# Kernel optimization log

Hardware: AMD Instinct MI355X
Metric: run time of the kernel (lower is better)

The kernel has to match this reference:

```python
import jax, jax.numpy as jnp
import numpy as np

RATIO, NH, NG, KS, RF, UP = 4, 2, 2, 3, 11.0, 2


def _cln(t, g, b):
    # channel-wise LayerNorm on NCHW (LayerNormProxy), eps=1e-5
    mu = t.mean(axis=1, keepdims=True)
    var = ((t - mu) ** 2).mean(axis=1, keepdims=True)
    return (t - mu) * jax.lax.rsqrt(var + 1e-5) * g[None, :, None, None] + b[None, :, None, None]


def _resize_ac(img, oH, oW):
    # bilinear resize, align_corners=True (F.interpolate)
    H, W = img.shape[-2], img.shape[-1]
    ys = jnp.arange(oH, dtype=img.dtype) * ((H - 1) / (oH - 1))
    y0 = jnp.clip(jnp.floor(ys), 0, H - 2).astype(jnp.int32)
    wy = ys - y0.astype(img.dtype)
    xs = jnp.arange(oW, dtype=img.dtype) * ((W - 1) / (oW - 1))
    x0 = jnp.clip(jnp.floor(xs), 0, W - 2).astype(jnp.int32)
    wx = xs - x0.astype(img.dtype)
    t = img[..., y0, :] * (1.0 - wy)[:, None] + img[..., y0 + 1, :] * wy[:, None]
    return t[..., x0] * (1.0 - wx) + t[..., x0 + 1] * wx


def _grid_sample(img, iy, ix):
    # bilinear grid_sample, padding_mode='zeros', align_corners=True
    # img [Bg,Cx,H,W]; iy,ix [Bg,N] unnormalized input-pixel coords
    H, W = img.shape[-2], img.shape[-1]
    def one(im, yy, xx):
        y0f, x0f = jnp.floor(yy), jnp.floor(xx)
        wy, wx = yy - y0f, xx - x0f
        y0, x0 = y0f.astype(jnp.int32), x0f.astype(jnp.int32)
        def gat(yi, xi):
            valid = ((yi >= 0) & (yi < H) & (xi >= 0) & (xi < W)).astype(im.dtype)
            return im[:, jnp.clip(yi, 0, H - 1), jnp.clip(xi, 0, W - 1)] * valid[None]
        return (gat(y0, x0) * ((1 - wy) * (1 - wx))[None]
                + gat(y0, x0 + 1) * ((1 - wy) * wx)[None]
                + gat(y0 + 1, x0) * (wy * (1 - wx))[None]
                + gat(y0 + 1, x0 + 1) * (wy * wx)[None])
    return jax.vmap(one)(img, iy, ix)


def _conv2d(x, w, groups=1):
    return jax.lax.conv_general_dilated(x, w, (1, 1), 'SAME', feature_group_count=groups,
                                        dimension_numbers=('NCHW', 'OIHW', 'NCHW'))


def _forward(x, ln_g, ln_b, Wq, Wk, dw_w, off_ln_g, off_ln_b, off_w, off_b, rpb):
    B, C, H, W = x.shape
    hidden = C // RATIO
    gc = hidden // NG
    c2 = hidden // NH          # attn_dim per head
    oH, oW = int(H * UP), int(W * UP)
    N1, n = oH * oW, KS * KS
    scale = c2 ** -0.5
    v = x
    xn = _cln(x, ln_g, ln_b)
    q = jnp.einsum('oc,bchw->bohw', Wq, xn)
    k = jnp.einsum('oc,bchw->bohw', Wk, xn)
    q = _resize_ac(q, oH, oW)                        # [B,hidden,oH,oW]
    # offset prediction
    q_off = q.reshape(B * NG, gc, oH, oW)
    t = _conv2d(q_off, dw_w, groups=gc)
    t = _cln(t, off_ln_g, off_ln_b)
    t = jax.nn.gelu(t, approximate=False)
    pred = _conv2d(t, off_w) + off_b[None, :, None, None]  # [Bg,2*ks^2,oH,oW]
    pad = (KS - 1) // 2
    rng = jnp.arange(-pad, pad + 1, dtype=x.dtype)
    base = jnp.stack(jnp.meshgrid(rng, rng, indexing='ij'), axis=-1)  # [KS,KS,2] (y,x)
    off = jnp.tanh(pred).reshape(B * NG, KS, KS, 2, oH, oW) * RF + base[None, :, :, :, None, None]
    py = off[:, :, :, 0] + jnp.arange(oH, dtype=x.dtype)[None, None, None, :, None]
    px = off[:, :, :, 1] + jnp.arange(oW, dtype=x.dtype)[None, None, None, None, :]
    # normalize over (oH-1,oW-1) then denormalize onto (H-1,W-1) input grid (align_corners)
    iy = (py * ((H - 1) / (oH - 1))).reshape(B * NG, -1)
    ix = (px * ((W - 1) / (oW - 1))).reshape(B * NG, -1)
    kg = k.reshape(B * NG, hidden // NG, H, W)
    vg = v.reshape(B * NG, C // NG, H, W)
    kf = _grid_sample(kg, iy, ix).reshape(B, NG, hidden // NG, n, oH, oW)
    vf = _grid_sample(vg, iy, ix).reshape(B, NG, C // NG, n, oH, oW)
    # -> [B, N1, n, g*c] -> [B, nh, N1, n, c]
    kf = kf.transpose(0, 4, 5, 3, 1, 2).reshape(B, N1, n, NH, hidden // NH).transpose(0, 3, 1, 2, 4)
    vf = vf.transpose(0, 4, 5, 3, 1, 2).reshape(B, N1, n, NH, C // NH).transpose(0, 3, 1, 2, 4)
    kf = kf + rpb                                     # relative position bias on K
    qh = q.reshape(B, NH, c2, N1).transpose(0, 1, 3, 2) * scale  # [B,nh,N1,c2]
    attn = jax.nn.softmax(jnp.einsum('bhnc,bhnkc->bhnk', qh, kf), axis=-1)
    out = jnp.einsum('bhnk,bhnkc->bhnc', attn, vf)    # [B,nh,N1,C/nh]
    return out.transpose(0, 1, 3, 2).reshape(B, C, oH, oW)


def setup_inputs() -> dict:
    key = jax.random.key(0)
    ks = jax.random.split(key, 8)
    B, C, H, W = 2, 256, 48, 48
    hidden = C // RATIO
    gc = hidden // NG
    c2 = hidden // NH
    f32 = jnp.float32
    return {
        'x': jax.random.normal(ks[0], (B, C, H, W), f32),
        'ln_g': jnp.ones((C,), f32),
        'ln_b': jnp.zeros((C,), f32),
        'Wq': jax.random.normal(ks[1], (hidden, C), f32) * 0.05,
        'Wk': jax.random.normal(ks[2], (hidden, C), f32) * 0.05,
        'dw_w': jax.random.normal(ks[3], (gc, 1, 3, 3), f32) * 0.1,
        'off_ln_g': jnp.ones((gc,), f32),
        'off_ln_b': jnp.zeros((gc,), f32),
        'off_w': jax.random.normal(ks[4], (2 * KS * KS, gc, 3, 3), f32) * 0.02,
        'off_b': jnp.zeros((2 * KS * KS,), f32),
        'rpb': jax.random.normal(ks[5], (1, NH, 1, KS * KS, c2), f32) * 0.02,
    }


def reference(x, ln_g, ln_b, Wq, Wk, dw_w, off_ln_g, off_ln_b, off_w, off_b, rpb):
    return _forward(x, ln_g, ln_b, Wq, Wk, dw_w, off_ln_g, off_ln_b, off_w, off_b, rpb)
```

## Files before the change

kernel.cpp:

```cpp
#include <hip/hip_runtime.h>
#include <hip/hip_fp16.h>
#include <cstdint>
#include <cmath>

#define NB 2
#define NC 256
#define HW 2304
#define HID 64
#define OH 96
#define OW 96
#define N1 9216
#define SCALE_ATTN 0.17677669529663689f
#define RESZ ((float)(47.0/95.0))

__device__ __host__ inline int ocb8(int w) { return w < 2 ? 3 * w : 6 + 2 * (w - 2); }
__device__ __host__ inline int cnt8(int w) { return w < 2 ? 3 : 2; }

__global__ void kA_prep(const float* __restrict__ x, const float* __restrict__ Wq,
                        const float* __restrict__ Wk, const float* __restrict__ off_w,
                        const float* __restrict__ dw_w, const float* __restrict__ off_b,
                        float* __restrict__ v_nhwc, float* __restrict__ WT4,
                        float* __restrict__ dwT, float* __restrict__ wg2,
                        float* __restrict__ bsg2) {
    int blk = blockIdx.x;
    if (blk < 1152) {
        int pt = blk % 72;
        int t2 = blk / 72;
        int ct = t2 & 3;
        int bg = t2 >> 2;
        int b = bg >> 1, g = bg & 1;
        __shared__ float tile[32][33];
        int tx = threadIdx.x & 31, row = threadIdx.x >> 5;
#pragma unroll
        for (int r = 0; r < 4; r++) {
            int c = ct * 32 + row + r * 8;
            tile[row + r * 8][tx] = x[((size_t)(b * 256 + g * 128 + c)) * HW + pt * 32 + tx];
        }
        __syncthreads();
#pragma unroll
        for (int r = 0; r < 4; r++) {
            int p = pt * 32 + row + r * 8;
            v_nhwc[((size_t)bg * HW + p) * 128 + ct * 32 + tx] = tile[tx][row + r * 8];
        }
    } else {
        int idx = (blk - 1152) * 256 + threadIdx.x;
        if (idx < 32768) {
            int c = idx >> 7, t = idx & 127;
            float v = (t < 64) ? Wq[t * 256 + c] : Wk[(t - 64) * 256 + c];
            WT4[(((size_t)(c >> 2) * 128) + t) * 4 + (c & 3)] = v;
        } else if (idx < 32768 + 288) {
            int i = idx - 32768;
            int wi = i >> 5, c = i & 31;
            dwT[i] = dw_w[c * 9 + wi];
        } else if (idx < 32768 + 288 + 8 * 288 * 3) {
            int i = idx - (32768 + 288);
            int w = i / 864, r = i - w * 864;
            int kk = r / 3, j = r - kk * 3;
            wg2[i] = (j < cnt8(w)) ? off_w[(ocb8(w) + j) * 288 + kk] : 0.f;
        } else if (idx < 32768 + 288 + 8 * 288 * 3 + 24) {
            int i = idx - (32768 + 288 + 8 * 288 * 3);
            int w = i / 3, j = i - w * 3;
            bsg2[i] = (j < cnt8(w)) ? off_b[ocb8(w) + j] : 0.f;
        }
    }
}

__global__ __launch_bounds__(256) void k1_ln_qk(const float* __restrict__ v_nhwc,
                         const float* __restrict__ ln_g, const float* __restrict__ ln_b,
                         const float* __restrict__ WT4,
                         float* __restrict__ q_pix, float* __restrict__ k_nhwc) {
    int blk = blockIdx.x;
    int tid = threadIdx.x;
    int wv = tid >> 6, lane = tid & 63;
    __shared__ float xs[4][256];
    {
        int pix = blk * 4 + wv;
        int b = pix / HW, p = pix - b * HW;
        int c0 = lane * 2;
        float2 u0 = *(const float2*)(v_nhwc + (((size_t)(b * 2 + 0) * HW) + p) * 128 + c0);
        float2 u1 = *(const float2*)(v_nhwc + (((size_t)(b * 2 + 1) * HW) + p) * 128 + c0);
        float s = u0.x + u0.y + u1.x + u1.y;
#pragma unroll
        for (int off = 1; off < 64; off <<= 1) s += __shfl_xor(s, off);
        float mu = s * (1.f / 256.f);
        float d0 = u0.x - mu, d1 = u0.y - mu, d2 = u1.x - mu, d3 = u1.y - mu;
        float q = d0 * d0 + d1 * d1 + d2 * d2 + d3 * d3;
#pragma unroll
        for (int off = 1; off < 64; off <<= 1) q += __shfl_xor(q, off);
        float rs = rsqrtf(q * (1.f / 256.f) + 1e-5f);
        float2 w0, w1;
        w0.x = d0 * rs * ln_g[c0] + ln_b[c0];
        w0.y = d1 * rs * ln_g[c0 + 1] + ln_b[c0 + 1];
        w1.x = d2 * rs * ln_g[128 + c0] + ln_b[128 + c0];
        w1.y = d3 * rs * ln_g[129 + c0] + ln_b[129 + c0];
        *(float2*)&xs[wv][c0] = w0;
        *(float2*)&xs[wv][128 + c0] = w1;
    }
    __syncthreads();
    int o = tid & 127, ph = tid >> 7;
    float a0 = 0.f, a1 = 0.f;
    const float4* wp = (const float4*)WT4 + o;
    const float4* xa = (const float4*)xs[ph * 2];
    const float4* xb4 = (const float4*)xs[ph * 2 + 1];
#pragma unroll 8
    for (int c4 = 0; c4 < 64; c4++) {
        float4 w = wp[(size_t)c4 * 128];
        float4 p0 = xa[c4], p1 = xb4[c4];
        a0 += w.x * p0.x + w.y * p0.y + w.z * p0.z + w.w * p0.w;
        a1 += w.x * p1.x + w.y * p1.y + w.z * p1.z + w.w * p1.w;
    }
#pragma unroll
    for (int k = 0; k < 2; k++) {
        int pix = blk * 4 + ph * 2 + k;
        int b = pix / HW, p = pix - b * HW;
        float a = k ? a1 : a0;
        if (o < 64) {
            q_pix[(((size_t)b * HW) + p) * 64 + o] = a;
        } else {
            int t = o - 64, g = t >> 5, c32 = t & 31;
            k_nhwc[(((size_t)(b * 2 + g) * HW) + p) * 32 + c32] = a;
        }
    }
}

__global__ __launch_bounds__(256) void k3_t(const float* __restrict__ q_pix,
                                            const float* __restrict__ dwT,
                                            const float* __restrict__ og,
                                            const float* __restrict__ ob,
                                            __half* __restrict__ tbuf_h) {
    int gid = blockIdx.x * 256 + threadIdx.x;
    int c = gid & 31;
    int p2 = gid >> 5;
    int bg = p2 / N1, p = p2 - bg * N1;
    int b = bg >> 1, g = bg & 1;
    int oy = p / OW, ox = p - oy * OW;
    const float* qb = q_pix + ((size_t)b * HW) * 64 + g * 32 + c;
    float acc = 0.f;
#pragma unroll
    for (int dy = -1; dy <= 1; dy++) {
        int yy = oy + dy;
        if ((unsigned)yy >= (unsigned)OH) continue;
        float ysf = yy * RESZ;
        int y0 = min((int)ysf, 46);
        float wy = ysf - (float)y0;
#pragma unroll
        for (int dx = -1; dx <= 1; dx++) {
            int xx = ox + dx;
            if ((unsigned)xx >= (unsigned)OW) continue;
            float xsf = xx * RESZ;
            int x0 = min((int)xsf, 46);
            float wx = xsf - (float)x0;
            int i00 = (y0 * 48 + x0) * 64;
            float q00 = qb[i00], q01 = qb[i00 + 64];
            float q10 = qb[i00 + 48 * 64], q11 = qb[i00 + 49 * 64];
            float qv = (q00 * (1.f - wy) + q10 * wy) * (1.f - wx)
                     + (q01 * (1.f - wy) + q11 * wy) * wx;
            acc += qv * dwT[((dy + 1) * 3 + dx + 1) * 32 + c];
        }
    }
    float s = acc;
#pragma unroll
    for (int off = 1; off < 32; off <<= 1) s += __shfl_xor(s, off);
    float mu = s * (1.f / 32.f);
    float d = acc - mu;
    float v = d * d;
#pragma unroll
    for (int off = 1; off < 32; off <<= 1) v += __shfl_xor(v, off);
    float rsv = rsqrtf(v * (1.f / 32.f) + 1e-5f);
    float t = d * rsv * og[c] + ob[c];
    float ge = 0.5f * t * (1.f + erff(t * 0.70710678118654752f));
    tbuf_h[(size_t)p2 * 32 + c] = __float2half(ge);
}

__global__ __launch_bounds__(512) void k4_pred(const __half* __restrict__ tbuf_h,
                                               const float* __restrict__ wg2,
                                               const float* __restrict__ bsg2,
                                               float* __restrict__ pred) {
    int blk = blockIdx.x;
    int bg = blk / 144, tile = blk - bg * 144;
    int ty0 = (tile / 12) * 8, tx0 = (tile % 12) * 8;
    int tid = threadIdx.x;
    __shared__ float ts[100 * 33];

    const __half* tb = tbuf_h + (size_t)bg * N1 * 32;
    for (int item = tid; item < 400; item += 512) {
        int pt = item >> 2, qg = item & 3;
        int hy = ty0 + pt / 10 - 1;
        int hx = tx0 + pt % 10 - 1;
        float4 raw = make_float4(0.f, 0.f, 0.f, 0.f);
        if ((unsigned)hy < (unsigned)OH && (unsigned)hx < (unsigned)OW)
            raw = *(const float4*)(tb + ((size_t)(hy * OW + hx)) * 32 + qg * 8);
        const __half2* h2 = (const __half2*)&raw;
        int base = pt * 33 + qg * 8;
#pragma unroll
        for (int i = 0; i < 4; i++) {
            float2 f = __half22float2(h2[i]);
            ts[base + i * 2] = f.x;
            ts[base + i * 2 + 1] = f.y;
        }
    }
    __syncthreads();

    int w = __builtin_amdgcn_readfirstlane(tid >> 6);
    int lane = tid & 63;
    int y = lane >> 3, x = lane & 7;
    int ocb = ocb8(w), cnt = cnt8(w);
    float acc[3];
#pragma unroll
    for (int j = 0; j < 3; j++) acc[j] = bsg2[w * 3 + j];
    const float* tsb = &ts[(y * 10 + x) * 33];
    const float* wgp = wg2 + (size_t)w * 864;
    const int kof[9] = {0, 33, 66, 330, 363, 396, 660, 693, 726};
    for (int ic = 0; ic < 32; ic++) {
#pragma unroll
        for (int k = 0; k < 9; k++) {
            float tv = tsb[kof[k] + ic];
            const float* wr = wgp + (ic * 9 + k) * 3;
#pragma unroll
            for (int j = 0; j < 3; j++) acc[j] += tv * wr[j];
        }
    }
    int p = (ty0 + y) * OW + tx0 + x;
    float* pp = pred + ((size_t)bg * N1 + p) * 18 + ocb;
#pragma unroll
    for (int j = 0; j < 3; j++)
        if (j < cnt) pp[j] = acc[j];
}

__global__ __launch_bounds__(256) void k5_attn(const float* __restrict__ pred,
                                               const float* __restrict__ q_pix,
                                               const float* __restrict__ k_nhwc,
                                               const float* __restrict__ v_nhwc,
                                               const float* __restrict__ rpb,
                                               float* __restrict__ out) {
    int tid = threadIdx.x;
    int wv = __builtin_amdgcn_readfirstlane(tid >> 6);
    int lane = tid & 63;
    int gp = blockIdx.x * 16;
    int bg = gp / N1, p0 = gp % N1;
    int b = bg >> 1, g = bg & 1;
    int pw = p0 + wv * 4;
    int oy = pw / OW, ox0 = pw % OW;

    __shared__ float4 wts[4][4][9];
    __shared__ int4   cof[4][4][9];
    __shared__ float  outb[4][4][128];

    if (lane < 36) {
        int px = lane / 9, j = lane % 9;
        int p = pw + px;
        int ky = j / 3, kx = j % 3;
        const float* pp = pred + ((size_t)bg * N1 + p) * 18;
        float pr0 = pp[j * 2];
        float pr1 = pp[j * 2 + 1];
        float th0 = 1.f - 2.f * __builtin_amdgcn_rcpf(__expf(2.f * pr0) + 1.f);
        float th1 = 1.f - 2.f * __builtin_amdgcn_rcpf(__expf(2.f * pr1) + 1.f);
        float py  = th0 * 11.0f + (float)(ky - 1) + (float)oy;
        float pxc = th1 * 11.0f + (float)(kx - 1) + (float)(ox0 + px);
        float iy = py * RESZ, ix = pxc * RESZ;
        float y0f = floorf(iy), x0f = floorf(ix);
        float wy = iy - y0f, wx = ix - x0f;
        int y0 = (int)y0f, x0 = (int)x0f;
        bool vy0 = (unsigned)y0 < 48u, vy1 = (unsigned)(y0 + 1) < 48u;
        bool vx0 = (unsigned)x0 < 48u, vx1 = (unsigned)(x0 + 1) < 48u;
        int y0c = min(max(y0, 0), 47), y1c = min(max(y0 + 1, 0), 47);
        int x0c = min(max(x0, 0), 47), x1c = min(max(x0 + 1, 0), 47);
        float4 w;
        w.x = (vy0 && vx0) ? (1.f - wy) * (1.f - wx) : 0.f;
        w.y = (vy0 && vx1) ? (1.f - wy) * wx : 0.f;
        w.z = (vy1 && vx0) ? wy * (1.f - wx) : 0.f;
        w.w = (vy1 && vx1) ? wy * wx : 0.f;
        wts[wv][px][j] = w;
        cof[wv][px][j] = make_int4(y0c * 48 + x0c, y0c * 48 + x1c,
                                   y1c * 48 + x0c, y1c * 48 + x1c);
    }
    __syncthreads();

    int c = lane & 31, h = lane >> 5;
    int c4 = (lane & 31) * 4;
    const float* kb = k_nhwc + (size_t)bg * HW * 32;
    const float* rb = rpb + (size_t)g * 288;
    const float* qb = q_pix + (size_t)b * HW * 64 + g * 32 + c;
    const float* vbase = v_nhwc + (size_t)bg * HW * 128;

    float ysf = oy * RESZ;
    int qy0 = min((int)ysf, 46);
    float qwy = ysf - (float)qy0;

    float rv[5];
#pragma unroll
    for (int jj = 0; jj < 5; jj++) {
        int j = jj * 2 + h;
        rv[jj] = (j < 9) ? rb[j * 32 + c] : 0.f;
    }

    float qv[4];
#pragma unroll
    for (int px = 0; px < 4; px++) {
        float xsf = (ox0 + px) * RESZ;
        int qx0 = min((int)xsf, 46);
        float qwx = xsf - (float)qx0;
        int qi = (qy0 * 48 + qx0) * 64;
        float q00 = qb[qi], q01 = qb[qi + 64];
        float q10 = qb[qi + 48 * 64], q11 = qb[qi + 49 * 64];
        qv[px] = ((q00 * (1.f - qwy) + q10 * qwy) * (1.f - qwx)
                + (q01 * (1.f - qwy) + q11 * qwy) * qwx) * SCALE_ATTN;
    }

    float s[4][5];
#pragma unroll
    for (int px = 0; px < 4; px++) {
#pragma unroll
        for (int jj = 0; jj < 5; jj++) {
            int j = jj * 2 + h;
            float partial = 0.f;
            if (j < 9) {
                float4 w = wts[wv][px][j];
                int4 co = cof[wv][px][j];
                float kv = w.x * kb[co.x * 32 + c] + w.y * kb[co.y * 32 + c]
                         + w.z * kb[co.z * 32 + c] + w.w * kb[co.w * 32 + c];
                partial = qv[px] * (kv + rv[jj]);
            }
#pragma unroll
            for (int off = 1; off < 32; off <<= 1) partial += __shfl_xor(partial, off);
            s[px][jj] = (j < 9) ? partial : -1e30f;
        }
    }

#pragma unroll
    for (int px = 0; px < 4; px++) {
        float m = s[px][0];
#pragma unroll
        for (int jj = 1; jj < 5; jj++) m = fmaxf(m, s[px][jj]);
        m = fmaxf(m, __shfl_xor(m, 32));
        float e[5];
        float sum = 0.f;
#pragma unroll
        for (int jj = 0; jj < 5; jj++) { e[jj] = __expf(s[px][jj] - m); sum += e[jj]; }
        sum += __shfl_xor(sum, 32);
        float inv = __builtin_amdgcn_rcpf(sum);
#pragma unroll
        for (int jj = 0; jj < 5; jj++) s[px][jj] = e[jj] * inv;
    }

    float4 acc[4];
#pragma unroll
    for (int px = 0; px < 4; px++) acc[px] = make_float4(0.f, 0.f, 0.f, 0.f);
#pragma unroll
    for (int px = 0; px < 4; px++) {
#pragma unroll
        for (int jj = 0; jj < 5; jj++) {
            int j = jj * 2 + h;
            if (j < 9) {
                float pj = s[px][jj];
                float4 w = wts[wv][px][j];
                int4 co = cof[wv][px][j];
                float4 a0 = *(const float4*)(vbase + (size_t)co.x * 128 + c4);
                float4 a1 = *(const float4*)(vbase + (size_t)co.y * 128 + c4);
                float4 a2 = *(const float4*)(vbase + (size_t)co.z * 128 + c4);
                float4 a3 = *(const float4*)(vbase + (size_t)co.w * 128 + c4);
                float f0 = w.x * pj, f1 = w.y * pj, f2 = w.z * pj, f3 = w.w * pj;
                acc[px].x += f0 * a0.x + f1 * a1.x + f2 * a2.x + f3 * a3.x;
                acc[px].y += f0 * a0.y + f1 * a1.y + f2 * a2.y + f3 * a3.y;
                acc[px].z += f0 * a0.z + f1 * a1.z + f2 * a2.z + f3 * a3.z;
                acc[px].w += f0 * a0.w + f1 * a1.w + f2 * a2.w + f3 * a3.w;
            }
        }
    }
#pragma unroll
    for (int px = 0; px < 4; px++) {
        acc[px].x += __shfl_xor(acc[px].x, 32);
        acc[px].y += __shfl_xor(acc[px].y, 32);
        acc[px].z += __shfl_xor(acc[px].z, 32);
        acc[px].w += __shfl_xor(acc[px].w, 32);
        if (lane < 32) *(float4*)&outb[wv][px][c4] = acc[px];
    }
    __syncthreads();

    if (tid < 128) {
        int ch = tid;
        float* op = out + ((size_t)b * NC + g * 128 + ch) * N1 + p0;
#pragma unroll
        for (int w2 = 0; w2 < 4; w2++) {
            float4 v4 = make_float4(outb[w2][0][ch], outb[w2][1][ch],
                                    outb[w2][2][ch], outb[w2][3][ch]);
            *(float4*)(op + w2 * 4) = v4;
        }
    }
}

extern "C" void kernel_launch(void* const* d_in, const int* in_sizes, int n_in,
                              void* d_out, int out_size, void* d_ws, size_t ws_size,
                              hipStream_t stream) {
    const float* x      = (const float*)d_in[0];
    const float* ln_g   = (const float*)d_in[1];
    const float* ln_b   = (const float*)d_in[2];
    const float* Wq     = (const float*)d_in[3];
    const float* Wk     = (const float*)d_in[4];
    const float* dw_w   = (const float*)d_in[5];
    const float* off_g  = (const float*)d_in[6];
    const float* off_bt = (const float*)d_in[7];
    const float* off_w  = (const float*)d_in[8];
    const float* off_b  = (const float*)d_in[9];
    const float* rpb    = (const float*)d_in[10];
    float* out = (float*)d_out;

    float* ws = (float*)d_ws;
    float* v_nhwc = ws;
    float* WT4    = v_nhwc + 1179648;
    float* k_nhwc = WT4 + 32768;
    float* q_pix  = k_nhwc + 294912;
    float* pred   = q_pix + 294912;
    float* dwT    = pred + 663552;
    float* wg2    = dwT + 288;
    float* bsg2   = wg2 + 6912;
    __half* tbuf_h = (__half*)(bsg2 + 24);

    kA_prep<<<1309, 256, 0, stream>>>(x, Wq, Wk, off_w, dw_w, off_b,
                                      v_nhwc, WT4, dwT, wg2, bsg2);
    k1_ln_qk<<<1152, 256, 0, stream>>>(v_nhwc, ln_g, ln_b, WT4, q_pix, k_nhwc);
    k3_t<<<4608, 256, 0, stream>>>(q_pix, dwT, off_g, off_bt, tbuf_h);
    k4_pred<<<576, 512, 0, stream>>>(tbuf_h, wg2, bsg2, pred);
    k5_attn<<<2304, 256, 0, stream>>>(pred, q_pix, k_nhwc, v_nhwc, rpb, out);
}
```

Measured before the change: 166.7 us.

## Store V and K intermediates in fp16 and accumulate attention output with half2 FMA

The transposed value tensor and the key tensor are now stored as fp16 instead of fp32, halving the bytes the LN/projection kernel and the attention kernel gather. The attention value accumulation uses packed half2 FMAs on the fp16 values, and the workspace layout is rearranged to hold the half buffers. This cuts gather bandwidth and ALU work but loses accuracy, since both V storage and accumulation are in fp16 and may break tolerance.

```diff
diff --git a/kernel.cpp b/kernel.cpp
--- a/kernel.cpp
+++ b/kernel.cpp
@@ -16,10 +16,12 @@
 __device__ __host__ inline int ocb8(int w) { return w < 2 ? 3 * w : 6 + 2 * (w - 2); }
 __device__ __host__ inline int cnt8(int w) { return w < 2 ? 3 : 2; }
 
+struct h4v { __half2 lo, hi; };
+
 __global__ void kA_prep(const float* __restrict__ x, const float* __restrict__ Wq,
                         const float* __restrict__ Wk, const float* __restrict__ off_w,
                         const float* __restrict__ dw_w, const float* __restrict__ off_b,
-                        float* __restrict__ v_nhwc, float* __restrict__ WT4,
+                        __half* __restrict__ v_nhwc, float* __restrict__ WT4,
                         float* __restrict__ dwT, float* __restrict__ wg2,
                         float* __restrict__ bsg2) {
     int blk = blockIdx.x;
@@ -40,7 +42,8 @@
 #pragma unroll
         for (int r = 0; r < 4; r++) {
             int p = pt * 32 + row + r * 8;
-            v_nhwc[((size_t)bg * HW + p) * 128 + ct * 32 + tx] = tile[tx][row + r * 8];
+            v_nhwc[((size_t)bg * HW + p) * 128 + ct * 32 + tx] =
+                __float2half(tile[tx][row + r * 8]);
         }
     } else {
         int idx = (blk - 1152) * 256 + threadIdx.x;
@@ -65,10 +68,10 @@
     }
 }
 
-__global__ __launch_bounds__(256) void k1_ln_qk(const float* __restrict__ v_nhwc,
+__global__ __launch_bounds__(256) void k1_ln_qk(const __half* __restrict__ v_nhwc,
                          const float* __restrict__ ln_g, const float* __restrict__ ln_b,
                          const float* __restrict__ WT4,
-                         float* __restrict__ q_pix, float* __restrict__ k_nhwc) {
+                         float* __restrict__ q_pix, __half* __restrict__ k_nhwc) {
     int blk = blockIdx.x;
     int tid = threadIdx.x;
     int wv = tid >> 6, lane = tid & 63;
@@ -77,8 +80,10 @@
         int pix = blk * 4 + wv;
         int b = pix / HW, p = pix - b * HW;
         int c0 = lane * 2;
-        float2 u0 = *(const float2*)(v_nhwc + (((size_t)(b * 2 + 0) * HW) + p) * 128 + c0);
-        float2 u1 = *(const float2*)(v_nhwc + (((size_t)(b * 2 + 1) * HW) + p) * 128 + c0);
+        __half2 h0 = *(const __half2*)(v_nhwc + (((size_t)(b * 2 + 0) * HW) + p) * 128 + c0);
+        __half2 h1 = *(const __half2*)(v_nhwc + (((size_t)(b * 2 + 1) * HW) + p) * 128 + c0);
+        float2 u0 = __half22float2(h0);
+        float2 u1 = __half22float2(h1);
         float s = u0.x + u0.y + u1.x + u1.y;
 #pragma unroll
         for (int off = 1; off < 64; off <<= 1) s += __shfl_xor(s, off);
@@ -118,7 +123,7 @@
             q_pix[(((size_t)b * HW) + p) * 64 + o] = a;
         } else {
             int t = o - 64, g = t >> 5, c32 = t & 31;
-            k_nhwc[(((size_t)(b * 2 + g) * HW) + p) * 32 + c32] = a;
+            k_nhwc[(((size_t)(b * 2 + g) * HW) + p) * 32 + c32] = __float2half(a);
         }
     }
 }
@@ -229,8 +234,8 @@
 
 __global__ __launch_bounds__(256) void k5_attn(const float* __restrict__ pred,
                                                const float* __restrict__ q_pix,
-                                               const float* __restrict__ k_nhwc,
-                                               const float* __restrict__ v_nhwc,
+                                               const __half* __restrict__ k_nhwc,
+                                               const __half* __restrict__ v_nhwc,
                                                const float* __restrict__ rpb,
                                                float* __restrict__ out) {
     int tid = threadIdx.x;
@@ -278,10 +283,10 @@
 
     int c = lane & 31, h = lane >> 5;
     int c4 = (lane & 31) * 4;
-    const float* kb = k_nhwc + (size_t)bg * HW * 32;
+    const __half* kb = k_nhwc + (size_t)bg * HW * 32;
     const float* rb = rpb + (size_t)g * 288;
     const float* qb = q_pix + (size_t)b * HW * 64 + g * 32 + c;
-    const float* vbase = v_nhwc + (size_t)bg * HW * 128;
+    const __half* vb = v_nhwc + (size_t)bg * HW * 128 + c4;
 
     float ysf = oy * RESZ;
     int qy0 = min((int)ysf, 46);
@@ -317,8 +322,10 @@
             if (j < 9) {
                 float4 w = wts[wv][px][j];
                 int4 co = cof[wv][px][j];
-                float kv = w.x * kb[co.x * 32 + c] + w.y * kb[co.y * 32 + c]
-                         + w.z * kb[co.z * 32 + c] + w.w * kb[co.w * 32 + c];
+                float kv = w.x * __half2float(kb[co.x * 32 + c])
+                         + w.y * __half2float(kb[co.y * 32 + c])
+                         + w.z * __half2float(kb[co.z * 32 + c])
+                         + w.w * __half2float(kb[co.w * 32 + c]);
                 partial = qv[px] * (kv + rv[jj]);
             }
 #pragma unroll
@@ -343,9 +350,12 @@
         for (int jj = 0; jj < 5; jj++) s[px][jj] = e[jj] * inv;
     }
 
-    float4 acc[4];
-#pragma unroll
-    for (int px = 0; px < 4; px++) acc[px] = make_float4(0.f, 0.f, 0.f, 0.f);
+    __half2 ac0[4], ac1[4];
+#pragma unroll
+    for (int px = 0; px < 4; px++) {
+        ac0[px] = __float2half2_rn(0.f);
+        ac1[px] = __float2half2_rn(0.f);
+    }
 #pragma unroll
     for (int px = 0; px < 4; px++) {
 #pragma unroll
@@ -355,25 +365,35 @@
                 float pj = s[px][jj];
                 float4 w = wts[wv][px][j];
                 int4 co = cof[wv][px][j];
-                float4 a0 = *(const float4*)(vbase + (size_t)co.x * 128 + c4);
-                float4 a1 = *(const float4*)(vbase + (size_t)co.y * 128 + c4);
-                float4 a2 = *(const float4*)(vbase + (size_t)co.z * 128 + c4);
-                float4 a3 = *(const float4*)(vbase + (size_t)co.w * 128 + c4);
-                float f0 = w.x * pj, f1 = w.y * pj, f2 = w.z * pj, f3 = w.w * pj;
-                acc[px].x += f0 * a0.x + f1 * a1.x + f2 * a2.x + f3 * a3.x;
-                acc[px].y += f0 * a0.y + f1 * a1.y + f2 * a2.y + f3 * a3.y;
-                acc[px].z += f0 * a0.z + f1 * a1.z + f2 * a2.z + f3 * a3.z;
-                acc[px].w += f0 * a0.w + f1 * a1.w + f2 * a2.w + f3 * a3.w;
+                h4v a0 = *(const h4v*)(vb + (size_t)co.x * 128);
+                h4v a1 = *(const h4v*)(vb + (size_t)co.y * 128);
+                h4v a2 = *(const h4v*)(vb + (size_t)co.z * 128);
+                h4v a3 = *(const h4v*)(vb + (size_t)co.w * 128);
+                __half2 f0 = __float2half2_rn(w.x * pj);
+                __half2 f1 = __float2half2_rn(w.y * pj);
+                __half2 f2 = __float2half2_rn(w.z * pj);
+                __half2 f3 = __float2half2_rn(w.w * pj);
+                ac0[px] = __hfma2(f0, a0.lo, ac0[px]);
+                ac1[px] = __hfma2(f0, a0.hi, ac1[px]);
+                ac0[px] = __hfma2(f1, a1.lo, ac0[px]);
+                ac1[px] = __hfma2(f1, a1.hi, ac1[px]);
+                ac0[px] = __hfma2(f2, a2.lo, ac0[px]);
+                ac1[px] = __hfma2(f2, a2.hi, ac1[px]);
+                ac0[px] = __hfma2(f3, a3.lo, ac0[px]);
+                ac1[px] = __hfma2(f3, a3.hi, ac1[px]);
             }
         }
     }
 #pragma unroll
     for (int px = 0; px < 4; px++) {
-        acc[px].x += __shfl_xor(acc[px].x, 32);
-        acc[px].y += __shfl_xor(acc[px].y, 32);
-        acc[px].z += __shfl_xor(acc[px].z, 32);
-        acc[px].w += __shfl_xor(acc[px].w, 32);
-        if (lane < 32) *(float4*)&outb[wv][px][c4] = acc[px];
+        float2 lo = __half22float2(ac0[px]);
+        float2 hi = __half22float2(ac1[px]);
+        float4 acc = make_float4(lo.x, lo.y, hi.x, hi.y);
+        acc.x += __shfl_xor(acc.x, 32);
+        acc.y += __shfl_xor(acc.y, 32);
+        acc.z += __shfl_xor(acc.z, 32);
+        acc.w += __shfl_xor(acc.w, 32);
+        if (lane < 32) *(float4*)&outb[wv][px][c4] = acc;
     }
     __syncthreads();
 
@@ -406,15 +426,15 @@
     float* out = (float*)d_out;
 
     float* ws = (float*)d_ws;
-    float* v_nhwc = ws;
-    float* WT4    = v_nhwc + 1179648;
-    float* k_nhwc = WT4 + 32768;
-    float* q_pix  = k_nhwc + 294912;
+    float* WT4    = ws;
+    float* q_pix  = WT4 + 32768;
     float* pred   = q_pix + 294912;
     float* dwT    = pred + 663552;
     float* wg2    = dwT + 288;
     float* bsg2   = wg2 + 6912;
-    __half* tbuf_h = (__half*)(bsg2 + 24);
+    __half* v_nhwc = (__half*)(bsg2 + 24);
+    __half* k_nhwc = v_nhwc + 1179648;
+    __half* tbuf_h = k_nhwc + 294912;
 
     kA_prep<<<1309, 256, 0, stream>>>(x, Wq, Wk, off_w, dw_w, off_b,
                                       v_nhwc, WT4, dwT, wg2, bsg2);
```

Result: no change. 163.9 us (-1.7%).
